# Kernel optimization log

Hardware: AMD Instinct MI355X
Metric: run time of the kernel (lower is better)

Reference implementation:

```python
import jax, jax.numpy as jnp
import numpy as np

N_NODES = 100000
N_EDGES = 1000000
N_GRAPHS = 64
IN_F, H_F, N_CLS = 64, 64, 16
N_RELS = 8
N_BASES = 8  # DGL default: num_bases = num_rels when None


def setup_inputs() -> dict:
    key = jax.random.key(0)
    ks = jax.random.split(key, 16)
    in_feat = jax.random.normal(ks[0], (N_NODES, IN_F), dtype=jnp.float32)
    src = jax.random.randint(ks[1], (N_EDGES,), 0, N_NODES)
    dst = jax.random.randint(ks[2], (N_EDGES,), 0, N_NODES)
    etypes = jax.random.randint(ks[3], (N_EDGES,), 0, N_RELS)
    graph_ids = jnp.sort(jax.random.randint(ks[4], (N_NODES,), 0, N_GRAPHS))
    s1 = 1.0 / np.sqrt(IN_F)
    s2 = 1.0 / np.sqrt(H_F)
    bases1 = jax.random.normal(ks[5], (N_BASES, IN_F, H_F), dtype=jnp.float32) * s1
    coeff1 = jax.random.normal(ks[6], (N_RELS, N_BASES), dtype=jnp.float32) * (1.0 / np.sqrt(N_BASES))
    wself1 = jax.random.normal(ks[7], (IN_F, H_F), dtype=jnp.float32) * s1
    bias1 = jnp.zeros((H_F,), dtype=jnp.float32)
    bases2 = jax.random.normal(ks[8], (N_BASES, H_F, N_CLS), dtype=jnp.float32) * s2
    coeff2 = jax.random.normal(ks[9], (N_RELS, N_BASES), dtype=jnp.float32) * (1.0 / np.sqrt(N_BASES))
    wself2 = jax.random.normal(ks[10], (H_F, N_CLS), dtype=jnp.float32) * s2
    bias2 = jnp.zeros((N_CLS,), dtype=jnp.float32)
    return {"in_feat": in_feat, "src": src, "dst": dst, "etypes": etypes,
            "graph_ids": graph_ids, "bases1": bases1, "coeff1": coeff1,
            "wself1": wself1, "bias1": bias1, "bases2": bases2,
            "coeff2": coeff2, "wself2": wself2, "bias2": bias2}


def _rel_graph_conv(x, src, dst, etypes, bases, coeff, wself, bias):
    # Basis decomposition: W_r = sum_b coeff[r,b] * bases[b]
    W = jnp.einsum('rb,bio->rio', coeff, bases)          # [R, in, out]
    # Project every node under every relation (R small), then gather per edge.
    xw = jnp.einsum('ni,rio->rno', x, W)                 # [R, N, out]
    msg = xw[etypes, src]                                 # [E, out]
    agg = jax.ops.segment_sum(msg, dst, num_segments=x.shape[0])
    # DGL defaults: self_loop=True, bias=True
    return agg + x @ wself + bias


def reference(in_feat, src, dst, etypes, graph_ids,
              bases1, coeff1, wself1, bias1,
              bases2, coeff2, wself2, bias2):
    h = _rel_graph_conv(in_feat, src, dst, etypes, bases1, coeff1, wself1, bias1)
    h = jax.nn.relu(h)
    h = _rel_graph_conv(h, src, dst, etypes, bases2, coeff2, wself2, bias2)
    h = jax.nn.relu(h)
    # dgl.mean_nodes: per-graph mean over node features
    sums = jax.ops.segment_sum(h, graph_ids, num_segments=N_GRAPHS)   # [G, C]
    counts = jax.ops.segment_sum(jnp.ones((h.shape[0],), h.dtype), graph_ids,
                                 num_segments=N_GRAPHS)
    return sums / jnp.maximum(counts, 1.0)[:, None]
```

## Files before the change

kernel.cpp:

```cpp
#include <hip/hip_runtime.h>


typedef __attribute__((ext_vector_type(8))) short bf16x8;
typedef __attribute__((ext_vector_type(4))) float f32x4;

#define NBLK 256

__device__ __forceinline__ unsigned short f2bf(float f) {
    unsigned u = __float_as_uint(f);
    unsigned r = u + 0x7FFFu + ((u >> 16) & 1u);
    return (unsigned short)(r >> 16);
}

__device__ __forceinline__ float bf2f(unsigned short u) {
    return __uint_as_float(((unsigned)u) << 16);
}

__device__ __forceinline__ unsigned pk2(float lo, float hi) {
    unsigned r;
    asm("v_cvt_pk_bf16_f32 %0, %1, %2" : "=v"(r) : "v"(lo), "v"(hi));
    return r;
}

union cv16 { uint4 u; bf16x8 b; };

__device__ __forceinline__ void acc8(uint4 m, float* a) {
    a[0] += bf2f((unsigned short)m.x); a[1] += bf2f((unsigned short)(m.x >> 16));
    a[2] += bf2f((unsigned short)m.y); a[3] += bf2f((unsigned short)(m.y >> 16));
    a[4] += bf2f((unsigned short)m.z); a[5] += bf2f((unsigned short)(m.z >> 16));
    a[6] += bf2f((unsigned short)m.w); a[7] += bf2f((unsigned short)(m.w >> 16));
}

__global__ __launch_bounds__(256) void k_bhist_w(
    const int* __restrict__ dst, int* __restrict__ bh, int nE, int nBins,
    const float* __restrict__ bases1, const float* __restrict__ coeff1,
    const float* __restrict__ bases2, const float* __restrict__ coeff2,
    const float* __restrict__ wself1, const float* __restrict__ wself2,
    unsigned short* __restrict__ W1f, unsigned short* __restrict__ W2f,
    unsigned short* __restrict__ W1sf, unsigned short* __restrict__ W2sf) {
    if (blockIdx.x >= NBLK) {
        int r = blockIdx.x - NBLK;
        int tid = threadIdx.x;
        float c1[8], c2[8];
#pragma unroll
        for (int b = 0; b < 8; ++b) { c1[b] = coeff1[r * 8 + b]; c2[b] = coeff2[r * 8 + b]; }
        for (int idx = tid; idx < 4096; idx += 256) {
            int j = idx & 7, lane = (idx >> 3) & 63, nt = (idx >> 9) & 3, kt = idx >> 11;
            int i = kt * 32 + ((lane >> 4) << 3) + j;
            int jo = nt * 16 + (lane & 15);
            float s = 0.f;
#pragma unroll
            for (int b = 0; b < 8; ++b) s = fmaf(c1[b], bases1[b * 4096 + i * 64 + jo], s);
            W1f[r * 4096 + idx] = f2bf(s);
            if (r == 0) W1sf[idx] = f2bf(wself1[i * 64 + jo]);
        }
        for (int idx = tid; idx < 1024; idx += 256) {
            int j = idx & 7, lane = (idx >> 3) & 63, kt = idx >> 9;
            int i = kt * 32 + ((lane >> 4) << 3) + j;
            int jo = lane & 15;
            float s = 0.f;
#pragma unroll
            for (int b = 0; b < 8; ++b) s = fmaf(c2[b], bases2[b * 1024 + i * 16 + jo], s);
            W2f[r * 1024 + idx] = f2bf(s);
            if (r == 0) W2sf[idx] = f2bf(wself2[i * 16 + jo]);
        }
        return;
    }
    __shared__ int h[512];
    for (int i = threadIdx.x; i < 512; i += 256) h[i] = 0;
    __syncthreads();
    int blk = blockIdx.x;
    int ech = (nE + NBLK - 1) / NBLK;
    int e0 = blk * ech, e1 = min(e0 + ech, nE);
    for (int e = e0 + threadIdx.x; e < e1; e += 256)
        atomicAdd(&h[dst[e] >> 8], 1);
    __syncthreads();
    for (int t = threadIdx.x; t < nBins; t += 256) bh[t * NBLK + blk] = h[t];
}

__global__ __launch_bounds__(256) void k_scanblk(
    const int* __restrict__ in, int* __restrict__ outx,
    int* __restrict__ btot, int n) {
    __shared__ int sm[256];
    int tid = threadIdx.x;
    int i = blockIdx.x * 256 + tid;
    int d = (i < n) ? in[i] : 0;
    sm[tid] = d;
    __syncthreads();
#pragma unroll
    for (int off = 1; off < 256; off <<= 1) {
        int v = (tid >= off) ? sm[tid - off] : 0;
        __syncthreads();
        sm[tid] += v;
        __syncthreads();
    }
    if (i < n) outx[i] = sm[tid] - d;
    if (tid == 255) btot[blockIdx.x] = sm[255];
}

__global__ void k_scantop(const int* __restrict__ btot, int* __restrict__ boff, int nB) {
    __shared__ int sm[512];
    int t = threadIdx.x;
    int d = (t < nB) ? btot[t] : 0;
    sm[t] = d;
    __syncthreads();
#pragma unroll
    for (int off = 1; off < 512; off <<= 1) {
        int v = (t >= off) ? sm[t - off] : 0;
        __syncthreads();
        sm[t] += v;
        __syncthreads();
    }
    if (t < nB) boff[t] = sm[t] - d;
}

__global__ __launch_bounds__(256) void k_scanadd2(
    int* __restrict__ bhs, const int* __restrict__ boff, int n) {
    int i = blockIdx.x * 256 + threadIdx.x;
    if (i < n) bhs[i] += boff[i >> 8];
}

__global__ __launch_bounds__(256) void k_bscat(
    const int* __restrict__ dst, const int* __restrict__ src,
    const int* __restrict__ et, const int* __restrict__ bhs,
    int* __restrict__ payload, int nE, int nBins) {
    __shared__ int cur[512];
    int blk = blockIdx.x;
    for (int t = threadIdx.x; t < nBins; t += 256) cur[t] = bhs[t * NBLK + blk];
    __syncthreads();
    int ech = (nE + NBLK - 1) / NBLK;
    int e0 = blk * ech, e1 = min(e0 + ech, nE);
    for (int e = e0 + threadIdx.x; e < e1; e += 256) {
        int d = dst[e];
        int pos = atomicAdd(&cur[d >> 8], 1);
        payload[pos] = ((src[e] * 9 + et[e]) << 8) | (d & 255);
    }
}

__global__ __launch_bounds__(256) void k_brefine(
    const int* __restrict__ payload, const int* __restrict__ bhs,
    int* __restrict__ skey, int* __restrict__ nodeoff,
    int nE, int nBins, int nNodes) {
    __shared__ int h[256];
    __shared__ int cur[256];
    __shared__ int sm[256];
    int b = blockIdx.x;
    int e0 = bhs[b * NBLK];
    int e1 = (b + 1 < nBins) ? bhs[(b + 1) * NBLK] : nE;
    int t = threadIdx.x;
    h[t] = 0;
    __syncthreads();
    for (int e = e0 + t; e < e1; e += 256)
        atomicAdd(&h[payload[e] & 255], 1);
    __syncthreads();
    int d = h[t];
    sm[t] = d;
    __syncthreads();
#pragma unroll
    for (int off = 1; off < 256; off <<= 1) {
        int v = (t >= off) ? sm[t - off] : 0;
        __syncthreads();
        sm[t] += v;
        __syncthreads();
    }
    int excl = sm[t] - d;
    cur[t] = excl;
    int n = (b << 8) + t;
    if (n < nNodes) nodeoff[n] = e0 + excl;
    __syncthreads();
    for (int e = e0 + t; e < e1; e += 256) {
        int pay = payload[e];
        int pos = atomicAdd(&cur[pay & 255], 1);
        skey[e0 + pos] = pay >> 8;
    }
    if (b == 0 && t == 0) nodeoff[nNodes] = nE;
}

#define XW1S 44
__global__ __launch_bounds__(256) void k_xw1(
    const float* __restrict__ x,
    const unsigned short* __restrict__ W1f,
    const unsigned short* __restrict__ W1sf,
    const float* __restrict__ bias1,
    unsigned short* __restrict__ xw1, int nNodes) {
    __shared__ unsigned lds[4][16 * XW1S];
    int lane = threadIdx.x & 63;
    int wid = (int)(threadIdx.x >> 6);
    int tile = blockIdx.x * 4 + wid;
    int n0 = tile * 16;
    if (n0 >= nNodes) return;
    int sA = n0 + (lane & 15);
    if (sA >= nNodes) sA = nNodes - 1;
    const float* xrow = x + (size_t)sA * 64 + ((lane >> 4) << 3);
    bf16x8 a[2];
#pragma unroll
    for (int kt = 0; kt < 2; ++kt) {
        f32x4 u0 = *(const f32x4*)(xrow + kt * 32);
        f32x4 u1 = *(const f32x4*)(xrow + kt * 32 + 4);
        cv16 c;
        c.u.x = pk2(u0[0], u0[1]);
        c.u.y = pk2(u0[2], u0[3]);
        c.u.z = pk2(u1[0], u1[1]);
        c.u.w = pk2(u1[2], u1[3]);
        a[kt] = c.b;
    }
    float bj[4];
#pragma unroll
    for (int nt = 0; nt < 4; ++nt) bj[nt] = bias1[nt * 16 + (lane & 15)];
    unsigned* L = lds[wid];
    const int even = !(lane & 1);
    const int cpair = (lane & 14) >> 1;
    int row2 = lane >> 2, ch = lane & 3;
    int nOut = n0 + row2;
    for (int r = 0; r < 9; ++r) {
        const unsigned short* Wf = (r < 8) ? (W1f + r * 4096) : W1sf;
        f32x4 z = {0.f, 0.f, 0.f, 0.f};
        f32x4 acc[4] = {z, z, z, z};
#pragma unroll
        for (int kt = 0; kt < 2; ++kt)
#pragma unroll
            for (int nt = 0; nt < 4; ++nt) {
                bf16x8 b = *(const bf16x8*)(Wf + (kt * 4 + nt) * 512 + lane * 8);
                acc[nt] = __builtin_amdgcn_mfma_f32_16x16x32_bf16(a[kt], b, acc[nt], 0, 0, 0);
            }
        if (r == 8) {
#pragma unroll
            for (int nt = 0; nt < 4; ++nt)
#pragma unroll
                for (int reg = 0; reg < 4; ++reg) acc[nt][reg] += bj[nt];
        }
#pragma unroll
        for (int reg = 0; reg < 4; ++reg) {
            int row = ((lane >> 4) << 2) + reg;
#pragma unroll
            for (int nt = 0; nt < 4; ++nt) {
                float mine = acc[nt][reg];
                float oth = __shfl_xor(mine, 1, 64);
                unsigned pk = even ? pk2(mine, oth) : pk2(oth, mine);
                if (even ? (nt < 2) : (nt >= 2)) L[row * XW1S + cpair + nt * 8] = pk;
            }
        }
        if (nOut < nNodes) {
            uint4 v0 = *(uint4*)&L[row2 * XW1S + ch * 4];
            uint4 v1 = *(uint4*)&L[row2 * XW1S + 16 + ch * 4];
            uint4* mp = (uint4*)(xw1 + ((size_t)nOut * 9 + r) * 64);
            mp[ch] = v0;
            mp[4 + ch] = v1;
        }
    }
}

__global__ __launch_bounds__(256) void k_f1(
    const unsigned short* __restrict__ xw1, const int* __restrict__ skey,
    const int* __restrict__ nodeoff,
    const unsigned short* __restrict__ W2f,
    const unsigned short* __restrict__ W2sf,
    const float* __restrict__ bias2,
    unsigned short* __restrict__ xw2, int nNodes) {
    __shared__ uint4 hbuf[64][9];
    __shared__ unsigned tlds[4][16 * 12];
    int t = threadIdx.x;
    int n0blk = blockIdx.x * 64;
    int gl = t & 7;
    int grp = t >> 3;
    for (int pass = 0; pass < 2; ++pass) {
        int nn = pass * 32 + grp;
        int n = n0blk + nn;
        uint4 p = {0, 0, 0, 0};
        if (n < nNodes) {
            int s0 = nodeoff[n], s1 = nodeoff[n + 1];
            uint4 v = *(const uint4*)(xw1 + ((size_t)n * 9 + 8) * 64 + gl * 8);
            float a[8];
            a[0] = bf2f((unsigned short)v.x); a[1] = bf2f((unsigned short)(v.x >> 16));
            a[2] = bf2f((unsigned short)v.y); a[3] = bf2f((unsigned short)(v.y >> 16));
            a[4] = bf2f((unsigned short)v.z); a[5] = bf2f((unsigned short)(v.z >> 16));
            a[6] = bf2f((unsigned short)v.w); a[7] = bf2f((unsigned short)(v.w >> 16));
            int i = s0;
            for (; i + 4 <= s1; i += 4) {
                int k0 = skey[i], k1 = skey[i + 1], k2 = skey[i + 2], k3 = skey[i + 3];
                uint4 m0 = *(const uint4*)(xw1 + (size_t)k0 * 64 + gl * 8);
                uint4 m1 = *(const uint4*)(xw1 + (size_t)k1 * 64 + gl * 8);
                uint4 m2 = *(const uint4*)(xw1 + (size_t)k2 * 64 + gl * 8);
                uint4 m3 = *(const uint4*)(xw1 + (size_t)k3 * 64 + gl * 8);
                acc8(m0, a); acc8(m1, a); acc8(m2, a); acc8(m3, a);
            }
            for (; i < s1; ++i) {
                uint4 m = *(const uint4*)(xw1 + (size_t)skey[i] * 64 + gl * 8);
                acc8(m, a);
            }
#pragma unroll
            for (int q = 0; q < 8; ++q) a[q] = fmaxf(a[q], 0.f);
            p.x = pk2(a[0], a[1]);
            p.y = pk2(a[2], a[3]);
            p.z = pk2(a[4], a[5]);
            p.w = pk2(a[6], a[7]);
        }
        hbuf[nn][gl] = p;
    }
    __syncthreads();
    int lane = t & 63;
    int w = t >> 6;
    int arow = w * 16 + (lane & 15);
    cv16 c0, c1;
    c0.u = hbuf[arow][lane >> 4];
    c1.u = hbuf[arow][4 + (lane >> 4)];
    bf16x8 a0 = c0.b, a1 = c1.b;
    float bj = bias2[lane & 15];
    unsigned* L = tlds[w];
    const int even = !(lane & 1);
    const int cpair = (lane & 14) >> 1;
    int row2 = lane >> 1, ch = lane & 1;
    int nOut = n0blk + w * 16 + row2;
    for (int r = 0; r < 9; ++r) {
        const unsigned short* Wf = (r < 8) ? (W2f + r * 1024) : W2sf;
        bf16x8 b0 = *(const bf16x8*)(Wf + lane * 8);
        bf16x8 b1 = *(const bf16x8*)(Wf + 512 + lane * 8);
        f32x4 acc = {0.f, 0.f, 0.f, 0.f};
        acc = __builtin_amdgcn_mfma_f32_16x16x32_bf16(a0, b0, acc, 0, 0, 0);
        acc = __builtin_amdgcn_mfma_f32_16x16x32_bf16(a1, b1, acc, 0, 0, 0);
        if (r == 8) {
#pragma unroll
            for (int reg = 0; reg < 4; ++reg) acc[reg] += bj;
        }
#pragma unroll
        for (int reg = 0; reg < 4; ++reg) {
            int row = ((lane >> 4) << 2) + reg;
            float mine = acc[reg];
            float oth = __shfl_xor(mine, 1, 64);
            unsigned pk = even ? pk2(mine, oth) : pk2(oth, mine);
            if (even ? (reg < 2) : (reg >= 2)) L[row * 12 + cpair] = pk;
        }
        if (lane < 32 && nOut < nNodes) {
            uint4 v = *(uint4*)&L[row2 * 12 + ch * 4];
            ((uint4*)(xw2 + ((size_t)nOut * 9 + r) * 16))[ch] = v;
        }
    }
}

__global__ __launch_bounds__(256) void k_seg2f(
    unsigned short* __restrict__ xw2, const int* __restrict__ skey,
    const int* __restrict__ nodeoff, int nNodes) {
    int gl = threadIdx.x & 1;
    int grp = (int)((blockIdx.x * blockDim.x + threadIdx.x) >> 1);
    int nG = (int)((gridDim.x * blockDim.x) >> 1);
    for (int n = grp; n < nNodes; n += nG) {
        int s0 = nodeoff[n], s1 = nodeoff[n + 1];
        uint4 v = *(const uint4*)(xw2 + ((size_t)n * 9 + 8) * 16 + gl * 8);
        float a[8];
        a[0] = bf2f((unsigned short)v.x); a[1] = bf2f((unsigned short)(v.x >> 16));
        a[2] = bf2f((unsigned short)v.y); a[3] = bf2f((unsigned short)(v.y >> 16));
        a[4] = bf2f((unsigned short)v.z); a[5] = bf2f((unsigned short)(v.z >> 16));
        a[6] = bf2f((unsigned short)v.w); a[7] = bf2f((unsigned short)(v.w >> 16));
        int i = s0;
        for (; i + 4 <= s1; i += 4) {
            int k0 = skey[i], k1 = skey[i + 1], k2 = skey[i + 2], k3 = skey[i + 3];
            uint4 m0 = *(const uint4*)(xw2 + (size_t)k0 * 16 + gl * 8);
            uint4 m1 = *(const uint4*)(xw2 + (size_t)k1 * 16 + gl * 8);
            uint4 m2 = *(const uint4*)(xw2 + (size_t)k2 * 16 + gl * 8);
            uint4 m3 = *(const uint4*)(xw2 + (size_t)k3 * 16 + gl * 8);
            acc8(m0, a); acc8(m1, a); acc8(m2, a); acc8(m3, a);
        }
        for (; i < s1; ++i) {
            uint4 m = *(const uint4*)(xw2 + (size_t)skey[i] * 16 + gl * 8);
            acc8(m, a);
        }
        uint4 p;
        p.x = pk2(a[0], a[1]);
        p.y = pk2(a[2], a[3]);
        p.z = pk2(a[4], a[5]);
        p.w = pk2(a[6], a[7]);
        *(uint4*)(xw2 + ((size_t)n * 9 + 8) * 16 + gl * 8) = p;
    }
}

__global__ __launch_bounds__(256) void k_pool(
    const unsigned short* __restrict__ xw2, const int* __restrict__ gid,
    float* __restrict__ out, int nNodes) {
    __shared__ float sm[256];
    __shared__ int bnd[2];
    int g = blockIdx.x;
    int t = threadIdx.x;
    if (t < 2) {
        int target = g + t;
        int lo = 0, hi = nNodes;
        while (lo < hi) {
            int mid = (lo + hi) >> 1;
            if (gid[mid] < target) lo = mid + 1; else hi = mid;
        }
        bnd[t] = lo;
    }
    __syncthreads();
    int s0 = bnd[0], s1 = bnd[1];
    int c = t & 15, idx = t >> 4;
    float acc = 0.f;
    for (int n = s0 + idx; n < s1; n += 16)
        acc += fmaxf(bf2f(xw2[((size_t)n * 9 + 8) * 16 + c]), 0.f);
    sm[t] = acc;
    __syncthreads();
#pragma unroll
    for (int off = 128; off >= 16; off >>= 1) {
        if (t < off) sm[t] += sm[t + off];
        __syncthreads();
    }
    if (t < 16) {
        float cnt = (float)(s1 - s0);
        out[g * 16 + t] = sm[t] / fmaxf(cnt, 1.f);
    }
}

extern "C" void kernel_launch(void* const* d_in, const int* in_sizes, int n_in,
                              void* d_out, int out_size, void* d_ws, size_t ws_size,
                              hipStream_t stream) {
    const float* x      = (const float*)d_in[0];
    const int*   src    = (const int*)d_in[1];
    const int*   dst    = (const int*)d_in[2];
    const int*   et     = (const int*)d_in[3];
    const int*   gid    = (const int*)d_in[4];
    const float* bases1 = (const float*)d_in[5];
    const float* coeff1 = (const float*)d_in[6];
    const float* wself1 = (const float*)d_in[7];
    const float* bias1  = (const float*)d_in[8];
    const float* bases2 = (const float*)d_in[9];
    const float* coeff2 = (const float*)d_in[10];
    const float* wself2 = (const float*)d_in[11];
    const float* bias2  = (const float*)d_in[12];
    float* out = (float*)d_out;

    int nNodes = in_sizes[0] / 64;
    int nE = in_sizes[1];
    int nBins = (nNodes + 255) >> 8;
    int nBh = nBins * NBLK;

    char* ws = (char*)d_ws;
    unsigned short* W1f  = (unsigned short*)(ws);
    unsigned short* W2f  = (unsigned short*)(ws + 65536);
    unsigned short* W1sf = (unsigned short*)(ws + 81920);
    unsigned short* W2sf = (unsigned short*)(ws + 90112);
    int*   payload = (int*)(ws + 92160);
    int*   skey    = (int*)(ws + 4092160);
    int*   nodeoff = (int*)(ws + 8092160);
    int*   bh      = (int*)(ws + 8492288);
    int*   bhs     = (int*)(ws + 8892672);
    int*   btot    = (int*)(ws + 9293056);
    int*   boff    = (int*)(ws + 9295104);
    unsigned short* xw1 = (unsigned short*)(ws + 9297152);
    unsigned short* xw2 = (unsigned short*)(ws + 124497152);

    int tiles = (nNodes + 15) / 16;
    int xwb = (tiles + 3) / 4;
    int f1b = (nNodes + 63) / 64;
    int scb = (nBh + 255) / 256;

    hipLaunchKernelGGL(k_bhist_w, dim3(NBLK + 8), dim3(256), 0, stream,
                       dst, bh, nE, nBins,
                       bases1, coeff1, bases2, coeff2, wself1, wself2,
                       W1f, W2f, W1sf, W2sf);
    hipLaunchKernelGGL(k_scanblk, dim3(scb), dim3(256), 0, stream,
                       bh, bhs, btot, nBh);
    hipLaunchKernelGGL(k_scantop, dim3(1), dim3(512), 0, stream, btot, boff, scb);
    hipLaunchKernelGGL(k_scanadd2, dim3(scb), dim3(256), 0, stream,
                       bhs, boff, nBh);
    hipLaunchKernelGGL(k_bscat, dim3(NBLK), dim3(256), 0, stream,
                       dst, src, et, bhs, payload, nE, nBins);
    hipLaunchKernelGGL(k_brefine, dim3(nBins), dim3(256), 0, stream,
                       payload, bhs, skey, nodeoff, nE, nBins, nNodes);
    hipLaunchKernelGGL(k_xw1, dim3(xwb), dim3(256), 0, stream,
                       x, W1f, W1sf, bias1, xw1, nNodes);
    hipLaunchKernelGGL(k_f1, dim3(f1b), dim3(256), 0, stream,
                       xw1, skey, nodeoff, W2f, W2sf, bias2, xw2, nNodes);
    hipLaunchKernelGGL(k_seg2f, dim3(1024), dim3(256), 0, stream,
                       xw2, skey, nodeoff, nNodes);
    hipLaunchKernelGGL(k_pool, dim3(64), dim3(256), 0, stream,
                       xw2, gid, out, nNodes);
}
```

Before: 177.1 us.

## Fuse bucket scatter with layer-1 projection and fold scan offset into consumers

Drops the separate scan-add kernel by adding the top-level block offsets inline wherever bin starts are read, in the scatter and in the refine kernel. Merges the edge bucket-scatter and the independent node projection GEMM into one launch, using block index ranges so the two workloads run concurrently on the GPU. This cuts two kernel launches and lets the memory-bound scatter overlap the projection compute. The merged kernel reserves shared memory for both roles, which may reduce occupancy.

```diff
diff --git a/kernel.cpp b/kernel.cpp
--- a/kernel.cpp
+++ b/kernel.cpp
@@ -114,79 +114,36 @@
     if (t < nB) boff[t] = sm[t] - d;
 }
 
-__global__ __launch_bounds__(256) void k_scanadd2(
-    int* __restrict__ bhs, const int* __restrict__ boff, int n) {
-    int i = blockIdx.x * 256 + threadIdx.x;
-    if (i < n) bhs[i] += boff[i >> 8];
-}
-
-__global__ __launch_bounds__(256) void k_bscat(
+#define XW1S 44
+__global__ __launch_bounds__(256) void k_mega(
     const int* __restrict__ dst, const int* __restrict__ src,
     const int* __restrict__ et, const int* __restrict__ bhs,
-    int* __restrict__ payload, int nE, int nBins) {
-    __shared__ int cur[512];
-    int blk = blockIdx.x;
-    for (int t = threadIdx.x; t < nBins; t += 256) cur[t] = bhs[t * NBLK + blk];
-    __syncthreads();
-    int ech = (nE + NBLK - 1) / NBLK;
-    int e0 = blk * ech, e1 = min(e0 + ech, nE);
-    for (int e = e0 + threadIdx.x; e < e1; e += 256) {
-        int d = dst[e];
-        int pos = atomicAdd(&cur[d >> 8], 1);
-        payload[pos] = ((src[e] * 9 + et[e]) << 8) | (d & 255);
-    }
-}
-
-__global__ __launch_bounds__(256) void k_brefine(
-    const int* __restrict__ payload, const int* __restrict__ bhs,
-    int* __restrict__ skey, int* __restrict__ nodeoff,
-    int nE, int nBins, int nNodes) {
-    __shared__ int h[256];
-    __shared__ int cur[256];
-    __shared__ int sm[256];
-    int b = blockIdx.x;
-    int e0 = bhs[b * NBLK];
-    int e1 = (b + 1 < nBins) ? bhs[(b + 1) * NBLK] : nE;
-    int t = threadIdx.x;
-    h[t] = 0;
-    __syncthreads();
-    for (int e = e0 + t; e < e1; e += 256)
-        atomicAdd(&h[payload[e] & 255], 1);
-    __syncthreads();
-    int d = h[t];
-    sm[t] = d;
-    __syncthreads();
-#pragma unroll
-    for (int off = 1; off < 256; off <<= 1) {
-        int v = (t >= off) ? sm[t - off] : 0;
-        __syncthreads();
-        sm[t] += v;
-        __syncthreads();
-    }
-    int excl = sm[t] - d;
-    cur[t] = excl;
-    int n = (b << 8) + t;
-    if (n < nNodes) nodeoff[n] = e0 + excl;
-    __syncthreads();
-    for (int e = e0 + t; e < e1; e += 256) {
-        int pay = payload[e];
-        int pos = atomicAdd(&cur[pay & 255], 1);
-        skey[e0 + pos] = pay >> 8;
-    }
-    if (b == 0 && t == 0) nodeoff[nNodes] = nE;
-}
-
-#define XW1S 44
-__global__ __launch_bounds__(256) void k_xw1(
+    const int* __restrict__ boff, int* __restrict__ payload,
+    int nE, int nBins,
     const float* __restrict__ x,
     const unsigned short* __restrict__ W1f,
     const unsigned short* __restrict__ W1sf,
     const float* __restrict__ bias1,
     unsigned short* __restrict__ xw1, int nNodes) {
+    __shared__ int cur[512];
     __shared__ unsigned lds[4][16 * XW1S];
+    if (blockIdx.x < NBLK) {
+        int blk = blockIdx.x;
+        for (int t = threadIdx.x; t < nBins; t += 256)
+            cur[t] = bhs[t * NBLK + blk] + boff[t];
+        __syncthreads();
+        int ech = (nE + NBLK - 1) / NBLK;
+        int e0 = blk * ech, e1 = min(e0 + ech, nE);
+        for (int e = e0 + threadIdx.x; e < e1; e += 256) {
+            int d = dst[e];
+            int pos = atomicAdd(&cur[d >> 8], 1);
+            payload[pos] = ((src[e] * 9 + et[e]) << 8) | (d & 255);
+        }
+        return;
+    }
     int lane = threadIdx.x & 63;
     int wid = (int)(threadIdx.x >> 6);
-    int tile = blockIdx.x * 4 + wid;
+    int tile = (blockIdx.x - NBLK) * 4 + wid;
     int n0 = tile * 16;
     if (n0 >= nNodes) return;
     int sA = n0 + (lane & 15);
@@ -248,6 +205,46 @@
             mp[4 + ch] = v1;
         }
     }
+}
+
+__global__ __launch_bounds__(256) void k_brefine(
+    const int* __restrict__ payload, const int* __restrict__ bhs,
+    const int* __restrict__ boff,
+    int* __restrict__ skey, int* __restrict__ nodeoff,
+    int nE, int nBins, int nNodes) {
+    __shared__ int h[256];
+    __shared__ int cur[256];
+    __shared__ int sm[256];
+    int b = blockIdx.x;
+    int e0 = bhs[b * NBLK] + boff[b];
+    int e1 = (b + 1 < nBins) ? (bhs[(b + 1) * NBLK] + boff[b + 1]) : nE;
+    int t = threadIdx.x;
+    h[t] = 0;
+    __syncthreads();
+    for (int e = e0 + t; e < e1; e += 256)
+        atomicAdd(&h[payload[e] & 255], 1);
+    __syncthreads();
+    int d = h[t];
+    sm[t] = d;
+    __syncthreads();
+#pragma unroll
+    for (int off = 1; off < 256; off <<= 1) {
+        int v = (t >= off) ? sm[t - off] : 0;
+        __syncthreads();
+        sm[t] += v;
+        __syncthreads();
+    }
+    int excl = sm[t] - d;
+    cur[t] = excl;
+    int n = (b << 8) + t;
+    if (n < nNodes) nodeoff[n] = e0 + excl;
+    __syncthreads();
+    for (int e = e0 + t; e < e1; e += 256) {
+        int pay = payload[e];
+        int pos = atomicAdd(&cur[pay & 255], 1);
+        skey[e0 + pos] = pay >> 8;
+    }
+    if (b == 0 && t == 0) nodeoff[nNodes] = nE;
 }
 
 __global__ __launch_bounds__(256) void k_f1(
@@ -458,14 +455,11 @@
     hipLaunchKernelGGL(k_scanblk, dim3(scb), dim3(256), 0, stream,
                        bh, bhs, btot, nBh);
     hipLaunchKernelGGL(k_scantop, dim3(1), dim3(512), 0, stream, btot, boff, scb);
-    hipLaunchKernelGGL(k_scanadd2, dim3(scb), dim3(256), 0, stream,
-                       bhs, boff, nBh);
-    hipLaunchKernelGGL(k_bscat, dim3(NBLK), dim3(256), 0, stream,
-                       dst, src, et, bhs, payload, nE, nBins);
+    hipLaunchKernelGGL(k_mega, dim3(NBLK + xwb), dim3(256), 0, stream,
+                       dst, src, et, bhs, boff, payload, nE, nBins,
+                       x, W1f, W1sf, bias1, xw1, nNodes);
     hipLaunchKernelGGL(k_brefine, dim3(nBins), dim3(256), 0, stream,
-                       payload, bhs, skey, nodeoff, nE, nBins, nNodes);
-    hipLaunchKernelGGL(k_xw1, dim3(xwb), dim3(256), 0, stream,
-                       x, W1f, W1sf, bias1, xw1, nNodes);
+                       payload, bhs, boff, skey, nodeoff, nE, nBins, nNodes);
     hipLaunchKernelGGL(k_f1, dim3(f1b), dim3(256), 0, stream,
                        xw1, skey, nodeoff, W2f, W2sf, bias2, xw2, nNodes);
     hipLaunchKernelGGL(k_seg2f, dim3(1024), dim3(256), 0, stream,
```

After: 167.4 us, median of 2. -5.5%, faster.
